# Kernel tuning notes

Measured on AMD Instinct MI355X. Metric: run time of the kernel, lower is better.

Reference implementation:

```python
import jax, jax.numpy as jnp
import numpy as np
import math

D_MODEL = 1024
N_HEADS = 16
D_K = 64
D_V = 64
B = 4
S = 1024


def setup_inputs() -> dict:
    key = jax.random.key(0)
    ks = jax.random.split(key, 11)
    # xavier-ish init scale for projections
    s_in = 1.0 / math.sqrt(D_MODEL)
    return {
        "queries": jax.random.normal(ks[0], (B, S, D_MODEL), jnp.float32),
        "keys": jax.random.normal(ks[1], (B, S, D_MODEL), jnp.float32),
        "values": jax.random.normal(ks[2], (B, S, D_MODEL), jnp.float32),
        "Wq": jax.random.normal(ks[3], (D_MODEL, N_HEADS * D_K), jnp.float32) * s_in,
        "bq": jnp.zeros((N_HEADS * D_K,), jnp.float32),
        "Wk": jax.random.normal(ks[4], (D_MODEL, N_HEADS * D_K), jnp.float32) * s_in,
        "bk": jnp.zeros((N_HEADS * D_K,), jnp.float32),
        "Wv": jax.random.normal(ks[5], (D_MODEL, N_HEADS * D_V), jnp.float32) * s_in,
        "bv": jnp.zeros((N_HEADS * D_V,), jnp.float32),
        "Wo": jax.random.normal(ks[6], (N_HEADS * D_V, D_MODEL), jnp.float32) * (1.0 / math.sqrt(N_HEADS * D_V)),
        "bo": jnp.zeros((D_MODEL,), jnp.float32),
    }


def reference(queries, keys, values, Wq, bq, Wk, bk, Wv, bv, Wo, bo):
    Bq, Sq, _ = queries.shape
    Sk = keys.shape[1]
    scale = 1.0 / math.sqrt(D_K)
    # projections -> [B, S, H, d]
    q = (queries @ Wq + bq).reshape(Bq, Sq, N_HEADS, D_K)
    k = (keys @ Wk + bk).reshape(Bq, Sk, N_HEADS, D_K)
    v = (values @ Wv + bv).reshape(Bq, Sk, N_HEADS, D_V)
    # scaled dot-product attention: scores [B, H, Sq, Sk]
    scores = jnp.einsum("bqhd,bkhd->bhqk", q, k) * scale
    attn = jax.nn.softmax(scores, axis=-1)
    # weighted values -> [B, Sq, H*D_V]
    out = jnp.einsum("bhqk,bkhd->bqhd", attn, v).reshape(Bq, Sq, N_HEADS * D_V)
    return out @ Wo + bo
```

## Files before the change

kernel.cpp:

```cpp
#include <hip/hip_runtime.h>
#include <hip/hip_bf16.h>

typedef __attribute__((ext_vector_type(4))) float f32x4;
typedef __attribute__((ext_vector_type(16))) float f32x16;
typedef __attribute__((ext_vector_type(8))) short bf16x8;
typedef __attribute__((ext_vector_type(4))) unsigned short u16x4;
typedef __attribute__((ext_vector_type(8))) unsigned short u16x8;
typedef __attribute__((ext_vector_type(2))) unsigned int u32x2;

#define MFMA16(a, b, c) __builtin_amdgcn_mfma_f32_16x16x32_bf16((a), (b), (c), 0, 0, 0)
#define MFMA32(a, b, c) __builtin_amdgcn_mfma_f32_32x32x16_bf16((a), (b), (c), 0, 0, 0)

static __device__ __forceinline__ unsigned short f2bf(float f) {
    union { float f; unsigned int u; } v; v.f = f;
    unsigned int r = v.u + 0x7FFFu + ((v.u >> 16) & 1u);
    return (unsigned short)(r >> 16);
}
static __device__ __forceinline__ unsigned int pk2(float x, float y) {
    unsigned int r;
    asm("v_cvt_pk_bf16_f32 %0, %1, %2" : "=v"(r) : "v"(x), "v"(y));
    return r;
}

static __device__ __forceinline__ void gload_lds16(const void* g, void* l) {
    __builtin_amdgcn_global_load_lds(
        (const __attribute__((address_space(1))) void*)g,
        (__attribute__((address_space(3))) void*)l, 16, 0, 0);
}

__global__ __launch_bounds__(256) void convert_act(
    const float* __restrict__ q, const float* __restrict__ k,
    const float* __restrict__ v, unsigned short* __restrict__ qc,
    unsigned short* __restrict__ kc, unsigned short* __restrict__ vc) {
    const float* src = blockIdx.y == 0 ? q : (blockIdx.y == 1 ? k : v);
    unsigned short* dst = blockIdx.y == 0 ? qc : (blockIdx.y == 1 ? kc : vc);
    size_t off = ((size_t)blockIdx.x * 256 + threadIdx.x) * 8;
    f32x4 a = *(const f32x4*)&src[off];
    f32x4 b = *(const f32x4*)&src[off + 4];
    union { unsigned int u[4]; u16x8 v; } o;
    o.u[0] = pk2(a[0], a[1]); o.u[1] = pk2(a[2], a[3]);
    o.u[2] = pk2(b[0], b[1]); o.u[3] = pk2(b[2], b[3]);
    *(u16x8*)&dst[off] = o.v;
}

__global__ __launch_bounds__(256) void transpose_w(
    const float* __restrict__ Wq, const float* __restrict__ Wk,
    const float* __restrict__ Wv, const float* __restrict__ Wo,
    unsigned short* __restrict__ Wt_all, unsigned short* __restrict__ Wot) {
    __shared__ unsigned short T[64][65];
    const int z = blockIdx.z;
    const float* W = z == 0 ? Wq : (z == 1 ? Wk : (z == 2 ? Wv : Wo));
    unsigned short* Wt = z < 3 ? (Wt_all + (size_t)z * 1024 * 1024) : Wot;
    const int k0 = blockIdx.y * 64, n0 = blockIdx.x * 64;
    const int t = threadIdx.x;
    const int rl = t >> 4, c4 = (t & 15) * 4;
#pragma unroll
    for (int i = 0; i < 4; ++i) {
        f32x4 v = *(const f32x4*)&W[(size_t)(k0 + rl + 16 * i) * 1024 + n0 + c4];
#pragma unroll
        for (int j = 0; j < 4; ++j) T[rl + 16 * i][c4 + j] = f2bf(v[j]);
    }
    __syncthreads();
#pragma unroll
    for (int i = 0; i < 4; ++i) {
        u16x4 o;
#pragma unroll
        for (int j = 0; j < 4; ++j) o[j] = T[c4 + j][rl + 16 * i];
        *(u16x4*)&Wt[(size_t)(n0 + rl + 16 * i) * 1024 + k0 + c4] = o;
    }
}

template <bool OUT_BF16, int BN>
__global__ __launch_bounds__(256, 2) void gemm_fast(
    const unsigned short* __restrict__ A0, const unsigned short* __restrict__ A1,
    const unsigned short* __restrict__ A2, const unsigned short* __restrict__ Wt,
    const float* __restrict__ b0, const float* __restrict__ b1,
    const float* __restrict__ b2, void* __restrict__ Outv, int ldo) {
    constexpr int NF = BN / 32;
    __shared__ __align__(16) unsigned short As[128 * 32];
    __shared__ __align__(16) unsigned short Bs[BN * 32];

    const int t = threadIdx.x;
    const int w = t >> 6, lane = t & 63;
    const int wr = w >> 1, wc = w & 1;
    const int g = lane >> 4, r15 = lane & 15;
    const int bm = blockIdx.y * 128;
    const int bn = blockIdx.x * BN;
    const int msel = bn >> 10;
    const unsigned short* A = msel == 0 ? A0 : (msel == 1 ? A1 : A2);
    const float* bias = msel == 0 ? b0 : (msel == 1 ? b1 : b2);
    const int l4 = lane >> 2, c8 = (lane & 3) * 8;

    f32x4 acc[4][NF];
#pragma unroll
    for (int m = 0; m < 4; ++m)
#pragma unroll
        for (int n = 0; n < NF; ++n) acc[m][n] = (f32x4){0.f, 0.f, 0.f, 0.f};

    for (int kt = 0; kt < 1024; kt += 32) {
        __syncthreads();
        gload_lds16(&A[(size_t)(bm + 16 * w + l4) * 1024 + kt + c8], &As[w * 512]);
        gload_lds16(&A[(size_t)(bm + 16 * (w + 4) + l4) * 1024 + kt + c8], &As[(w + 4) * 512]);
        if (BN == 128) {
            gload_lds16(&Wt[(size_t)(bn + 16 * w + l4) * 1024 + kt + c8], &Bs[w * 512]);
            gload_lds16(&Wt[(size_t)(bn + 16 * (w + 4) + l4) * 1024 + kt + c8],
                        &Bs[(w + 4) * 512 % (BN * 32)]);
        } else {
            gload_lds16(&Wt[(size_t)(bn + 16 * w + l4) * 1024 + kt + c8], &Bs[w * 512]);
        }
        __syncthreads();
        bf16x8 af[4], bfr[NF];
#pragma unroll
        for (int m = 0; m < 4; ++m)
            af[m] = *(const bf16x8*)&As[(wr * 64 + m * 16 + r15) * 32 + g * 8];
#pragma unroll
        for (int n = 0; n < NF; ++n)
            bfr[n] = *(const bf16x8*)&Bs[(wc * (BN / 2) + n * 16 + r15) * 32 + g * 8];
#pragma unroll
        for (int m = 0; m < 4; ++m)
#pragma unroll
            for (int n = 0; n < NF; ++n)
                acc[m][n] = MFMA16(af[m], bfr[n], acc[m][n]);
    }

    float* Of = (float*)Outv;
    unsigned short* Ob = (unsigned short*)Outv;
#pragma unroll
    for (int n = 0; n < NF; ++n) {
        int col = bn + wc * (BN / 2) + n * 16 + r15;
        float bv = bias[col & 1023];
#pragma unroll
        for (int m = 0; m < 4; ++m) {
#pragma unroll
            for (int r = 0; r < 4; ++r) {
                int row = bm + wr * 64 + m * 16 + g * 4 + r;
                float val = acc[m][n][r] + bv;
                if (OUT_BF16)
                    Ob[(size_t)row * ldo + col] = f2bf(val);
                else
                    Of[(size_t)row * ldo + col] = val;
            }
        }
    }
}

template <bool A_BF16, bool OUT_BF16>
__global__ __launch_bounds__(256, 2) void gemm_kernel(
    const void* __restrict__ Av, const float* __restrict__ W,
    const float* __restrict__ bias, void* __restrict__ Outv) {
    __shared__ __align__(16) unsigned short As[128][40];
    __shared__ __align__(16) unsigned short Bs[128][40];

    const int t = threadIdx.x;
    const int bm = blockIdx.y * 128;
    const int bn = blockIdx.x * 128;
    const int w = t >> 6, lane = t & 63;
    const int wr = w >> 1, wc = w & 1;
    const int g = lane >> 4, r15 = lane & 15;

    f32x4 acc[4][4];
#pragma unroll
    for (int m = 0; m < 4; ++m)
#pragma unroll
        for (int n = 0; n < 4; ++n) acc[m][n] = (f32x4){0.f, 0.f, 0.f, 0.f};

    const float* Af = (const float*)Av;
    const unsigned short* Ab = (const unsigned short*)Av;

    for (int kt = 0; kt < 1024; kt += 32) {
        __syncthreads();
#pragma unroll
        for (int i = 0; i < 4; ++i) {
            int row = (t >> 3) + i * 32;
            int c4 = (t & 7) * 4;
            if (A_BF16) {
                u16x4 v = *(const u16x4*)&Ab[(size_t)(bm + row) * 1024 + kt + c4];
                *(u16x4*)&As[row][c4] = v;
            } else {
                f32x4 v = *(const f32x4*)&Af[(size_t)(bm + row) * 1024 + kt + c4];
                u16x4 o;
                o[0] = f2bf(v[0]); o[1] = f2bf(v[1]);
                o[2] = f2bf(v[2]); o[3] = f2bf(v[3]);
                *(u16x4*)&As[row][c4] = o;
            }
        }
#pragma unroll
        for (int i = 0; i < 4; ++i) {
            int k = (t >> 5) + i * 8;
            int c4 = (t & 31) * 4;
            f32x4 v = *(const f32x4*)&W[(size_t)(kt + k) * 1024 + bn + c4];
#pragma unroll
            for (int j = 0; j < 4; ++j) Bs[c4 + j][k] = f2bf(v[j]);
        }
        __syncthreads();
        bf16x8 af[4], bfr[4];
#pragma unroll
        for (int m = 0; m < 4; ++m)
            af[m] = *(const bf16x8*)&As[wr * 64 + m * 16 + r15][g * 8];
#pragma unroll
        for (int n = 0; n < 4; ++n)
            bfr[n] = *(const bf16x8*)&Bs[wc * 64 + n * 16 + r15][g * 8];
#pragma unroll
        for (int m = 0; m < 4; ++m)
#pragma unroll
            for (int n = 0; n < 4; ++n)
                acc[m][n] = MFMA16(af[m], bfr[n], acc[m][n]);
    }

    float* Of = (float*)Outv;
    unsigned short* Ob = (unsigned short*)Outv;
#pragma unroll
    for (int n = 0; n < 4; ++n) {
        int col = bn + wc * 64 + n * 16 + r15;
        float bv = bias[col];
#pragma unroll
        for (int m = 0; m < 4; ++m) {
#pragma unroll
            for (int r = 0; r < 4; ++r) {
                int row = bm + wr * 64 + m * 16 + g * 4 + r;
                float val = acc[m][n][r] + bv;
                if (OUT_BF16)
                    Ob[(size_t)row * 1024 + col] = f2bf(val);
                else
                    Of[(size_t)row * 1024 + col] = val;
            }
        }
    }
}

__global__ __launch_bounds__(256, 2) void attn32_kernel(
    const unsigned short* __restrict__ Q, const unsigned short* __restrict__ K,
    const unsigned short* __restrict__ V, unsigned short* __restrict__ O, int ld) {
    __shared__ __align__(16) unsigned short Kls[2][64 * 80];
    __shared__ __align__(16) unsigned short Vls[2][64 * 80];

    const int t = threadIdx.x;
    const int w = t >> 6, lane = t & 63;
    const int q5 = lane & 31, hi = lane >> 5;

    const int id = blockIdx.x;
    const int sid = (id & 7) * 64 + (id >> 3);
    const int bh = sid >> 3, qb = sid & 7;
    const int b = bh >> 4, h = bh & 15;
    const int brow = b * 1024;
    const int q0 = qb * 128;

    const float c2 = 0.18033688f;

    const unsigned short* Qrow = Q + (size_t)(brow + q0 + w * 32 + q5) * ld + h * 64;
    bf16x8 qreg[8];
#pragma unroll
    for (int j = 0; j < 8; ++j) qreg[j] = *(const bf16x8*)&Qrow[8 * j];
    bf16x8 qsel[4];
#pragma unroll
    for (int kk = 0; kk < 4; ++kk) qsel[kk] = hi ? qreg[2 * kk + 1] : qreg[2 * kk];

    const int krow = t >> 2, kpart = t & 3;
    const int vp = t & 31, vdc = t >> 5;
    const unsigned short* Kg = K + h * 64;
    const unsigned short* Vg = V + h * 64;

    u16x8 kr0, kr1, vr0, vr1;
#define STG_LOAD(KT)                                                            \
    {                                                                           \
        size_t kro = (size_t)(brow + (KT) + krow) * ld;                         \
        kr0 = *(const u16x8*)&Kg[kro + kpart * 8];                              \
        kr1 = *(const u16x8*)&Kg[kro + kpart * 8 + 32];                         \
        size_t vro = (size_t)(brow + (KT) + 2 * vp) * ld;                       \
        vr0 = *(const u16x8*)&Vg[vro + vdc * 8];                                \
        vr1 = *(const u16x8*)&Vg[vro + ld + vdc * 8];                           \
    }
#define STG_WRITE(BUF)                                                          \
    {                                                                           \
        char* kb_ = (char*)Kls[BUF];                                            \
        int tg_ = (krow & 7) << 4;                                              \
        *(u16x8*)(kb_ + krow * 160 + ((kpart * 16) ^ tg_)) = kr0;               \
        *(u16x8*)(kb_ + krow * 160 + (((kpart + 4) * 16) ^ tg_)) = kr1;         \
        char* vb_ = (char*)Vls[BUF];                                            \
        _Pragma("unroll") for (int j_ = 0; j_ < 8; ++j_) {                      \
            int d_ = vdc * 8 + j_;                                              \
            unsigned int pk_ = (unsigned int)(unsigned short)vr0[j_] |          \
                               ((unsigned int)(unsigned short)vr1[j_] << 16);   \
            *(unsigned int*)(vb_ + d_ * 160 + ((vp * 4) ^ ((d_ & 7) << 4)))     \
                = pk_;                                                          \
        }                                                                       \
    }

    f32x16 acc0 = {}, acc1 = {};
    float mrun = -1e30f, lrun = 0.f;

    STG_LOAD(0);
    STG_WRITE(0);
    __syncthreads();

    int cur = 0;
    for (int tile = 0; tile < 16; ++tile) {
        const bool more = tile < 15;
        if (more) STG_LOAD(tile * 64 + 64);

        char* kb = (char*)Kls[cur];
        f32x16 st0 = {}, st1 = {};
        {
            const int tg0 = (q5 & 7) << 4;
            char* kp0 = kb + q5 * 160;
            char* kp1 = kb + (q5 + 32) * 160;
            __builtin_amdgcn_s_setprio(1);
#pragma unroll
            for (int kk = 0; kk < 4; ++kk) {
                int so = ((2 * kk + hi) * 16) ^ tg0;
                bf16x8 kf0 = *(const bf16x8*)(kp0 + so);
                bf16x8 kf1 = *(const bf16x8*)(kp1 + so);
                st0 = MFMA32(kf0, qsel[kk], st0);
                st1 = MFMA32(kf1, qsel[kk], st1);
            }
            __builtin_amdgcn_s_setprio(0);
        }

        float mloc = fmaxf(st0[0], st0[1]);
#pragma unroll
        for (int r = 2; r < 16; ++r) mloc = fmaxf(mloc, st0[r]);
#pragma unroll
        for (int r = 0; r < 16; ++r) mloc = fmaxf(mloc, st1[r]);
        mloc = fmaxf(mloc, __shfl_xor(mloc, 32));
        if (!__all(mloc - mrun <= 64.f)) {
            float mnew = fmaxf(mrun, mloc);
            float sf = exp2f((mrun - mnew) * c2);
            mrun = mnew;
            lrun *= sf;
#pragma unroll
            for (int r = 0; r < 16; ++r) { acc0[r] *= sf; acc1[r] *= sf; }
        }
        float mneg = -mrun * c2;
        float rs = 0.f;
#pragma unroll
        for (int r = 0; r < 16; ++r) {
            st0[r] = exp2f(fmaf(st0[r], c2, mneg));
            rs += st0[r];
        }
#pragma unroll
        for (int r = 0; r < 16; ++r) {
            st1[r] = exp2f(fmaf(st1[r], c2, mneg));
            rs += st1[r];
        }
        rs += __shfl_xor(rs, 32);
        lrun += rs;

        char* vb = (char*)Vls[cur];
        const int tgv = (q5 & 7) << 4;
        char* vp0 = vb + q5 * 160;
        char* vp1 = vb + (q5 + 32) * 160;
        __builtin_amdgcn_s_setprio(1);
#define PV_HALF(ST, CT)                                                         \
    _Pragma("unroll") for (int ks = 0; ks < 2; ++ks) {                          \
        unsigned int a0 = pk2(ST[8 * ks + 0], ST[8 * ks + 1]);                  \
        unsigned int a1 = pk2(ST[8 * ks + 2], ST[8 * ks + 3]);                  \
        unsigned int a2 = pk2(ST[8 * ks + 4], ST[8 * ks + 5]);                  \
        unsigned int a3 = pk2(ST[8 * ks + 6], ST[8 * ks + 7]);                  \
        unsigned int x0 = __shfl_xor(a0, 32), x1 = __shfl_xor(a1, 32);          \
        unsigned int x2 = __shfl_xor(a2, 32), x3 = __shfl_xor(a3, 32);          \
        union { unsigned int u[4]; bf16x8 v; } pfu;                             \
        pfu.u[0] = hi ? x2 : a0;                                                \
        pfu.u[1] = hi ? x3 : a1;                                                \
        pfu.u[2] = hi ? a2 : x0;                                                \
        pfu.u[3] = hi ? a3 : x1;                                                \
        int co = ((32 * (2 * (CT) + ks) + 16 * hi)) ^ tgv;                      \
        bf16x8 vf0 = *(const bf16x8*)(vp0 + co);                                \
        bf16x8 vf1 = *(const bf16x8*)(vp1 + co);                                \
        acc0 = MFMA32(vf0, pfu.v, acc0);                                        \
        acc1 = MFMA32(vf1, pfu.v, acc1);                                        \
    }
        PV_HALF(st0, 0);
        PV_HALF(st1, 1);
        __builtin_amdgcn_s_setprio(0);

        if (more) STG_WRITE(cur ^ 1);
        __syncthreads();
        cur ^= 1;
    }

    const float inv = 1.0f / lrun;
    unsigned short* Orow = O + (size_t)(brow + q0 + w * 32 + q5) * 1024 + h * 64;
#pragma unroll
    for (int k = 0; k < 4; ++k) {
        int d0 = 8 * k + 4 * hi;
        u32x2 pa, pb;
        pa[0] = pk2(acc0[4 * k + 0] * inv, acc0[4 * k + 1] * inv);
        pa[1] = pk2(acc0[4 * k + 2] * inv, acc0[4 * k + 3] * inv);
        *(u32x2*)&Orow[d0] = pa;
        pb[0] = pk2(acc1[4 * k + 0] * inv, acc1[4 * k + 1] * inv);
        pb[1] = pk2(acc1[4 * k + 2] * inv, acc1[4 * k + 3] * inv);
        *(u32x2*)&Orow[32 + d0] = pb;
    }
#undef STG_LOAD
#undef STG_WRITE
#undef PV_HALF
}

extern "C" void kernel_launch(void* const* d_in, const int* in_sizes, int n_in,
                              void* d_out, int out_size, void* d_ws, size_t ws_size,
                              hipStream_t stream) {
    const float* q  = (const float*)d_in[0];
    const float* k  = (const float*)d_in[1];
    const float* v  = (const float*)d_in[2];
    const float* Wq = (const float*)d_in[3];
    const float* bq = (const float*)d_in[4];
    const float* Wk = (const float*)d_in[5];
    const float* bk = (const float*)d_in[6];
    const float* Wv = (const float*)d_in[7];
    const float* bv = (const float*)d_in[8];
    const float* Wo = (const float*)d_in[9];
    const float* bo = (const float*)d_in[10];

    const size_t M1 = (size_t)1024 * 1024;
    const size_t NEED = 28 * M1 * sizeof(unsigned short);

    dim3 bt(256, 1, 1);
    if (ws_size >= NEED) {
        unsigned short* qc  = (unsigned short*)d_ws;
        unsigned short* kc  = qc + 4 * M1;
        unsigned short* vc  = kc + 4 * M1;
        unsigned short* Wt  = vc + 4 * M1;
        unsigned short* Wot = Wt + 3 * M1;
        unsigned short* QKV = Wot + M1;
        unsigned short* Ob  = qc;

        convert_act<<<dim3(2048, 3), bt, 0, stream>>>(q, k, v, qc, kc, vc);
        transpose_w<<<dim3(16, 16, 4), bt, 0, stream>>>(Wq, Wk, Wv, Wo, Wt, Wot);
        gemm_fast<true, 128><<<dim3(24, 32), bt, 0, stream>>>(qc, kc, vc, Wt, bq, bk, bv, QKV, 3072);
        attn32_kernel<<<dim3(512), bt, 0, stream>>>(QKV, QKV + 1024, QKV + 2048, Ob, 3072);
        gemm_fast<false, 64><<<dim3(16, 32), bt, 0, stream>>>(Ob, Ob, Ob, Wot, bo, bo, bo, d_out, 1024);
    } else {
        const size_t NE = (size_t)4096 * 1024;
        unsigned short* Qb = (unsigned short*)d_ws;
        unsigned short* Kb = Qb + NE;
        unsigned short* Vb = Kb + NE;
        unsigned short* Ob = Vb + NE;
        dim3 gg(8, 32);
        gemm_kernel<false, true><<<gg, bt, 0, stream>>>(q, Wq, bq, Qb);
        gemm_kernel<false, true><<<gg, bt, 0, stream>>>(k, Wk, bk, Kb);
        gemm_kernel<false, true><<<gg, bt, 0, stream>>>(v, Wv, bv, Vb);
        attn32_kernel<<<dim3(512), bt, 0, stream>>>(Qb, Kb, Vb, Ob, 1024);
        gemm_kernel<true, false><<<gg, bt, 0, stream>>>(Ob, Wo, bo, d_out);
    }
}
```

Measured before the change: 217.6 us.

## Split attention KV range across wave pairs and double-buffer GEMM LDS stages

```diff
diff --git a/kernel.cpp b/kernel.cpp
--- a/kernel.cpp
+++ b/kernel.cpp
@@ -77,8 +77,8 @@
     const float* __restrict__ b0, const float* __restrict__ b1,
     const float* __restrict__ b2, void* __restrict__ Outv, int ldo) {
     constexpr int NF = BN / 32;
-    __shared__ __align__(16) unsigned short As[128 * 32];
-    __shared__ __align__(16) unsigned short Bs[BN * 32];
+    __shared__ __align__(16) unsigned short As[2][128 * 32];
+    __shared__ __align__(16) unsigned short Bs[2][BN * 32];
 
     const int t = threadIdx.x;
     const int w = t >> 6, lane = t & 63;
@@ -97,31 +97,47 @@
 #pragma unroll
         for (int n = 0; n < NF; ++n) acc[m][n] = (f32x4){0.f, 0.f, 0.f, 0.f};
 
+#define G_STAGE(BUF, KT)                                                          \
+    {                                                                             \
+        gload_lds16(&A[(size_t)(bm + 16 * w + l4) * 1024 + (KT) + c8],            \
+                    &As[BUF][w * 512]);                                           \
+        gload_lds16(&A[(size_t)(bm + 16 * (w + 4) + l4) * 1024 + (KT) + c8],      \
+                    &As[BUF][(w + 4) * 512]);                                     \
+        if (BN == 128) {                                                          \
+            gload_lds16(&Wt[(size_t)(bn + 16 * w + l4) * 1024 + (KT) + c8],       \
+                        &Bs[BUF][(w * 512) % (BN * 32)]);                         \
+            gload_lds16(&Wt[(size_t)(bn + 16 * (w + 4) + l4) * 1024 + (KT) + c8], \
+                        &Bs[BUF][((w + 4) * 512) % (BN * 32)]);                   \
+        } else if (w < 4) {                                                       \
+            gload_lds16(&Wt[(size_t)(bn + 16 * w + l4) * 1024 + (KT) + c8],       \
+                        &Bs[BUF][(w * 512) % (BN * 32)]);                         \
+        }                                                                         \
+    }
+
+    G_STAGE(0, 0);
+    __syncthreads();
+
+    int cur = 0;
     for (int kt = 0; kt < 1024; kt += 32) {
-        __syncthreads();
-        gload_lds16(&A[(size_t)(bm + 16 * w + l4) * 1024 + kt + c8], &As[w * 512]);
-        gload_lds16(&A[(size_t)(bm + 16 * (w + 4) + l4) * 1024 + kt + c8], &As[(w + 4) * 512]);
-        if (BN == 128) {
-            gload_lds16(&Wt[(size_t)(bn + 16 * w + l4) * 1024 + kt + c8], &Bs[w * 512]);
-            gload_lds16(&Wt[(size_t)(bn + 16 * (w + 4) + l4) * 1024 + kt + c8],
-                        &Bs[(w + 4) * 512 % (BN * 32)]);
-        } else {
-            gload_lds16(&Wt[(size_t)(bn + 16 * w + l4) * 1024 + kt + c8], &Bs[w * 512]);
-        }
-        __syncthreads();
+        if (kt < 992) G_STAGE(cur ^ 1, kt + 32);
         bf16x8 af[4], bfr[NF];
 #pragma unroll
         for (int m = 0; m < 4; ++m)
-            af[m] = *(const bf16x8*)&As[(wr * 64 + m * 16 + r15) * 32 + g * 8];
+            af[m] = *(const bf16x8*)&As[cur][(wr * 64 + m * 16 + r15) * 32 + g * 8];
 #pragma unroll
         for (int n = 0; n < NF; ++n)
-            bfr[n] = *(const bf16x8*)&Bs[(wc * (BN / 2) + n * 16 + r15) * 32 + g * 8];
+            bfr[n] = *(const bf16x8*)&Bs[cur][(wc * (BN / 2) + n * 16 + r15) * 32 + g * 8];
+        __builtin_amdgcn_s_setprio(1);
 #pragma unroll
         for (int m = 0; m < 4; ++m)
 #pragma unroll
             for (int n = 0; n < NF; ++n)
                 acc[m][n] = MFMA16(af[m], bfr[n], acc[m][n]);
-    }
+        __builtin_amdgcn_s_setprio(0);
+        __syncthreads();
+        cur ^= 1;
+    }
+#undef G_STAGE
 
     float* Of = (float*)Outv;
     unsigned short* Ob = (unsigned short*)Outv;
@@ -228,7 +244,7 @@
     }
 }
 
-__global__ __launch_bounds__(256, 2) void attn32_kernel(
+__global__ __launch_bounds__(256, 4) void attn32_kernel(
     const unsigned short* __restrict__ Q, const unsigned short* __restrict__ K,
     const unsigned short* __restrict__ V, unsigned short* __restrict__ O, int ld) {
     __shared__ __align__(16) unsigned short Kls[2][64 * 80];
@@ -237,17 +253,18 @@
     const int t = threadIdx.x;
     const int w = t >> 6, lane = t & 63;
     const int q5 = lane & 31, hi = lane >> 5;
+    const int wq = w & 1, wp = w >> 1;
 
     const int id = blockIdx.x;
-    const int sid = (id & 7) * 64 + (id >> 3);
-    const int bh = sid >> 3, qb = sid & 7;
+    const int sid = (id & 7) * 128 + (id >> 3);
+    const int bh = sid >> 4, qb = sid & 15;
     const int b = bh >> 4, h = bh & 15;
     const int brow = b * 1024;
-    const int q0 = qb * 128;
+    const int q0 = qb * 64;
 
     const float c2 = 0.18033688f;
 
-    const unsigned short* Qrow = Q + (size_t)(brow + q0 + w * 32 + q5) * ld + h * 64;
+    const unsigned short* Qrow = Q + (size_t)(brow + q0 + wq * 32 + q5) * ld + h * 64;
     bf16x8 qreg[8];
 #pragma unroll
     for (int j = 0; j < 8; ++j) qreg[j] = *(const bf16x8*)&Qrow[8 * j];
@@ -260,45 +277,55 @@
     const unsigned short* Kg = K + h * 64;
     const unsigned short* Vg = V + h * 64;
 
-    u16x8 kr0, kr1, vr0, vr1;
-#define STG_LOAD(KT)                                                            \
+    u16x8 krA0, krA1, krB0, krB1, vrA0, vrA1, vrB0, vrB1;
+#define STG_LOAD2(T)                                                            \
     {                                                                           \
-        size_t kro = (size_t)(brow + (KT) + krow) * ld;                         \
-        kr0 = *(const u16x8*)&Kg[kro + kpart * 8];                              \
-        kr1 = *(const u16x8*)&Kg[kro + kpart * 8 + 32];                         \
-        size_t vro = (size_t)(brow + (KT) + 2 * vp) * ld;                       \
-        vr0 = *(const u16x8*)&Vg[vro + vdc * 8];                                \
-        vr1 = *(const u16x8*)&Vg[vro + ld + vdc * 8];                           \
-    }
-#define STG_WRITE(BUF)                                                          \
+        size_t kroA = (size_t)(brow + (T) + krow) * ld;                         \
+        krA0 = *(const u16x8*)&Kg[kroA + kpart * 8];                            \
+        krA1 = *(const u16x8*)&Kg[kroA + kpart * 8 + 32];                       \
+        size_t kroB = (size_t)(brow + (T) + 64 + krow) * ld;                    \
+        krB0 = *(const u16x8*)&Kg[kroB + kpart * 8];                            \
+        krB1 = *(const u16x8*)&Kg[kroB + kpart * 8 + 32];                       \
+        size_t vroA = (size_t)(brow + (T) + 2 * vp) * ld;                       \
+        vrA0 = *(const u16x8*)&Vg[vroA + vdc * 8];                              \
+        vrA1 = *(const u16x8*)&Vg[vroA + ld + vdc * 8];                         \
+        size_t vroB = (size_t)(brow + (T) + 64 + 2 * vp) * ld;                  \
+        vrB0 = *(const u16x8*)&Vg[vroB + vdc * 8];                              \
+        vrB1 = *(const u16x8*)&Vg[vroB + ld + vdc * 8];                         \
+    }
+#define STG_W1(BUF, KR0, KR1, VR0, VR1)                                         \
     {                                                                           \
         char* kb_ = (char*)Kls[BUF];                                            \
         int tg_ = (krow & 7) << 4;                                              \
-        *(u16x8*)(kb_ + krow * 160 + ((kpart * 16) ^ tg_)) = kr0;               \
-        *(u16x8*)(kb_ + krow * 160 + (((kpart + 4) * 16) ^ tg_)) = kr1;         \
+        *(u16x8*)(kb_ + krow * 160 + ((kpart * 16) ^ tg_)) = KR0;               \
+        *(u16x8*)(kb_ + krow * 160 + (((kpart + 4) * 16) ^ tg_)) = KR1;         \
         char* vb_ = (char*)Vls[BUF];                                            \
         _Pragma("unroll") for (int j_ = 0; j_ < 8; ++j_) {                      \
             int d_ = vdc * 8 + j_;                                              \
-            unsigned int pk_ = (unsigned int)(unsigned short)vr0[j_] |          \
-                               ((unsigned int)(unsigned short)vr1[j_] << 16);   \
+            unsigned int pk_ = (unsigned int)(unsigned short)VR0[j_] |          \
+                               ((unsigned int)(unsigned short)VR1[j_] << 16);   \
             *(unsigned int*)(vb_ + d_ * 160 + ((vp * 4) ^ ((d_ & 7) << 4)))     \
                 = pk_;                                                          \
         }                                                                       \
     }
+#define STG_WRITE2()                          \
+    {                                         \
+        STG_W1(0, krA0, krA1, vrA0, vrA1);    \
+        STG_W1(1, krB0, krB1, vrB0, vrB1);    \
+    }
 
     f32x16 acc0 = {}, acc1 = {};
     float mrun = -1e30f, lrun = 0.f;
 
-    STG_LOAD(0);
-    STG_WRITE(0);
+    STG_LOAD2(0);
+    STG_WRITE2();
     __syncthreads();
 
-    int cur = 0;
-    for (int tile = 0; tile < 16; ++tile) {
-        const bool more = tile < 15;
-        if (more) STG_LOAD(tile * 64 + 64);
-
-        char* kb = (char*)Kls[cur];
+    for (int it = 0; it < 8; ++it) {
+        const bool more = it < 7;
+        if (more) STG_LOAD2(it * 128 + 128);
+
+        char* kb = (char*)Kls[wp];
         f32x16 st0 = {}, st1 = {};
         {
             const int tg0 = (q5 & 7) << 4;
@@ -345,7 +372,7 @@
         rs += __shfl_xor(rs, 32);
         lrun += rs;
 
-        char* vb = (char*)Vls[cur];
+        char* vb = (char*)Vls[wp];
         const int tgv = (q5 & 7) << 4;
         char* vp0 = vb + q5 * 160;
         char* vp1 = vb + (q5 + 32) * 160;
@@ -373,26 +400,54 @@
         PV_HALF(st1, 1);
         __builtin_amdgcn_s_setprio(0);
 
-        if (more) STG_WRITE(cur ^ 1);
-        __syncthreads();
-        cur ^= 1;
-    }
-
-    const float inv = 1.0f / lrun;
-    unsigned short* Orow = O + (size_t)(brow + q0 + w * 32 + q5) * 1024 + h * 64;
-#pragma unroll
-    for (int k = 0; k < 4; ++k) {
-        int d0 = 8 * k + 4 * hi;
-        u32x2 pa, pb;
-        pa[0] = pk2(acc0[4 * k + 0] * inv, acc0[4 * k + 1] * inv);
-        pa[1] = pk2(acc0[4 * k + 2] * inv, acc0[4 * k + 3] * inv);
-        *(u32x2*)&Orow[d0] = pa;
-        pb[0] = pk2(acc1[4 * k + 0] * inv, acc1[4 * k + 1] * inv);
-        pb[1] = pk2(acc1[4 * k + 2] * inv, acc1[4 * k + 3] * inv);
-        *(u32x2*)&Orow[32 + d0] = pb;
-    }
-#undef STG_LOAD
-#undef STG_WRITE
+        if (more) {
+            __syncthreads();
+            STG_WRITE2();
+            __syncthreads();
+        }
+    }
+
+    float* MG = (float*)Kls;
+    const int slot = (wq * 64 + lane) * 35;
+    __syncthreads();
+    if (wp == 1) {
+        MG[slot] = mrun;
+        MG[slot + 1] = lrun;
+#pragma unroll
+        for (int r = 0; r < 16; ++r) {
+            MG[slot + 2 + r] = acc0[r];
+            MG[slot + 18 + r] = acc1[r];
+        }
+    }
+    __syncthreads();
+    if (wp == 0) {
+        float m1 = MG[slot], l1 = MG[slot + 1];
+        float mn = fmaxf(mrun, m1);
+        float fa = exp2f((mrun - mn) * c2);
+        float fb = exp2f((m1 - mn) * c2);
+        float inv = 1.0f / (lrun * fa + l1 * fb);
+        fa *= inv; fb *= inv;
+        unsigned short* Orow =
+            O + (size_t)(brow + q0 + wq * 32 + q5) * 1024 + h * 64;
+#pragma unroll
+        for (int k = 0; k < 4; ++k) {
+            int d0 = 8 * k + 4 * hi;
+            u32x2 pa, pb;
+            pa[0] = pk2(acc0[4 * k + 0] * fa + MG[slot + 2 + 4 * k + 0] * fb,
+                        acc0[4 * k + 1] * fa + MG[slot + 2 + 4 * k + 1] * fb);
+            pa[1] = pk2(acc0[4 * k + 2] * fa + MG[slot + 2 + 4 * k + 2] * fb,
+                        acc0[4 * k + 3] * fa + MG[slot + 2 + 4 * k + 3] * fb);
+            *(u32x2*)&Orow[d0] = pa;
+            pb[0] = pk2(acc1[4 * k + 0] * fa + MG[slot + 18 + 4 * k + 0] * fb,
+                        acc1[4 * k + 1] * fa + MG[slot + 18 + 4 * k + 1] * fb);
+            pb[1] = pk2(acc1[4 * k + 2] * fa + MG[slot + 18 + 4 * k + 2] * fb,
+                        acc1[4 * k + 3] * fa + MG[slot + 18 + 4 * k + 3] * fb);
+            *(u32x2*)&Orow[32 + d0] = pb;
+        }
+    }
+#undef STG_LOAD2
+#undef STG_W1
+#undef STG_WRITE2
 #undef PV_HALF
 }
 
@@ -427,7 +482,7 @@
         convert_act<<<dim3(2048, 3), bt, 0, stream>>>(q, k, v, qc, kc, vc);
         transpose_w<<<dim3(16, 16, 4), bt, 0, stream>>>(Wq, Wk, Wv, Wo, Wt, Wot);
         gemm_fast<true, 128><<<dim3(24, 32), bt, 0, stream>>>(qc, kc, vc, Wt, bq, bk, bv, QKV, 3072);
-        attn32_kernel<<<dim3(512), bt, 0, stream>>>(QKV, QKV + 1024, QKV + 2048, Ob, 3072);
+        attn32_kernel<<<dim3(1024), bt, 0, stream>>>(QKV, QKV + 1024, QKV + 2048, Ob, 3072);
         gemm_fast<false, 64><<<dim3(16, 32), bt, 0, stream>>>(Ob, Ob, Ob, Wot, bo, bo, bo, d_out, 1024);
     } else {
         const size_t NE = (size_t)4096 * 1024;
@@ -439,7 +494,7 @@
         gemm_kernel<false, true><<<gg, bt, 0, stream>>>(q, Wq, bq, Qb);
         gemm_kernel<false, true><<<gg, bt, 0, stream>>>(k, Wk, bk, Kb);
         gemm_kernel<false, true><<<gg, bt, 0, stream>>>(v, Wv, bv, Vb);
-        attn32_kernel<<<dim3(512), bt, 0, stream>>>(Qb, Kb, Vb, Ob, 1024);
+        attn32_kernel<<<dim3(1024), bt, 0, stream>>>(Qb, Kb, Vb, Ob, 1024);
         gemm_kernel<true, false><<<gg, bt, 0, stream>>>(Ob, Wo, bo, d_out);
     }
 }
```

Result: slower. 275.3 us (+26.5%).
